# Kernel tuning notes

Hardware: AMD Instinct MI355X
Metric: run time of the kernel (lower is better)

## Reference

```python
import jax, jax.numpy as jnp
import numpy as np

DIM=2048; NH=16; QK_NOPE=128; QK_ROPE=64; QK_HD=QK_NOPE+QK_ROPE; V_HD=128
Q_LORA=1536; KV_LORA=512
IDX_NH=16; IDX_HD=128; IDX_TOPK=1024
B=1; S=2048
NEG=-1e30  # finite stand-in for -inf mask

def _hadamard(n):
    H=np.array([[1.0]],dtype=np.float32)
    while H.shape[0]<n:
        H=np.block([[H,H],[H,-H]])
    return H
_H=jnp.asarray(_hadamard(IDX_HD),jnp.bfloat16)  # symmetric Sylvester Hadamard

def _rope_tables(s,d):
    inv=1.0/(10000.0**(np.arange(0,d,2)/float(d)))
    ang=np.outer(np.arange(s),inv)
    return jnp.asarray(np.cos(ang),jnp.float32),jnp.asarray(np.sin(ang),jnp.float32)

def _rope_interleaved(x,cos,sin):
    # pairs (x[2i], x[2i+1]); x: (b,s,h,d), cos/sin: (s,d//2)
    x1=x[...,0::2]; x2=x[...,1::2]
    c=cos[None,:,None,:]; s_=sin[None,:,None,:]
    return jnp.stack([x1*c-x2*s_,x1*s_+x2*c],axis=-1).reshape(x.shape)

def _rope_half(x,cos,sin):
    # non-interleaved: pairs (x[i], x[i+d/2])
    d=x.shape[-1]//2
    x1=x[...,:d]; x2=x[...,d:]
    c=cos[None,:,None,:]; s_=sin[None,:,None,:]
    return jnp.concatenate([x1*c-x2*s_,x1*s_+x2*c],axis=-1)

def _rms(x,w,eps=1e-6):
    xf=x.astype(jnp.float32)
    xf=xf*jax.lax.rsqrt(jnp.mean(xf*xf,axis=-1,keepdims=True)+eps)
    return (w*xf).astype(x.dtype)

def _ln(x,w,b,eps=1e-6):
    xf=x.astype(jnp.float32)
    mu=jnp.mean(xf,axis=-1,keepdims=True)
    var=jnp.mean((xf-mu)**2,axis=-1,keepdims=True)
    return ((xf-mu)*jax.lax.rsqrt(var+eps)*w+b).astype(x.dtype)

def _rotate(x):
    # rotate_activation: bf16 Hadamard transform, x @ H * d^-0.5 (H symmetric)
    return (x.astype(jnp.bfloat16)@_H)*(IDX_HD**-0.5)

def _forward(x,start_pos,freqs_cos,freqs_sin,mask,q_a_proj,q_a_ln_w,q_b_proj,kv_a_proj,kv_a_ln_w,kv_b_proj,o_proj,idx_wq_b,idx_wk,idx_knorm_w,idx_knorm_b,idx_weights_proj):
    b,s,_=x.shape  # start_pos==0 prefill -> cache slice == current k/kv
    sm_scale=QK_HD**-0.5
    qr=_rms(x@q_a_proj.T,q_a_ln_w)                       # (b,s,q_lora)
    q=(qr@q_b_proj.T).reshape(b,s,NH,QK_HD)
    q_nope=q[...,:QK_NOPE]
    q_pe=_rope_interleaved(q[...,QK_NOPE:],freqs_cos,freqs_sin)
    kvp=x@kv_a_proj.T
    kv=_rms(kvp[...,:KV_LORA],kv_a_ln_w)                 # latent kv cache (b,t,c)
    k_pe=_rope_interleaved(kvp[...,KV_LORA:][:,:,None,:],freqs_cos,freqs_sin)[:,:,0,:]
    # ---------- Indexer ----------
    iq=(qr@idx_wq_b.T).reshape(b,s,IDX_NH,IDX_HD)
    iq=jnp.concatenate([_rope_half(iq[...,:QK_ROPE],freqs_cos,freqs_sin),iq[...,QK_ROPE:]],axis=-1)
    ik=_ln(x@idx_wk.T,idx_knorm_w,idx_knorm_b)           # (b,s,IDX_HD)
    ik=jnp.concatenate([_rope_half(ik[:,:,None,:QK_ROPE],freqs_cos,freqs_sin)[:,:,0,:],ik[...,QK_ROPE:]],axis=-1)
    iq=_rotate(iq); ik=_rotate(ik)                       # bf16 Hadamard-rotated
    iw=(x@idx_weights_proj.T)*(IDX_NH**-0.5)             # (b,s,hI)
    wq=(iw[...,None]*iq.astype(jnp.float32)*(IDX_HD**-0.5)).astype(jnp.bfloat16)
    sc=jnp.einsum('bshd,btd->bsht',wq,ik,preferred_element_type=jnp.float32)
    index_score=jax.nn.relu(sc).sum(axis=2)+mask[None]   # bf16_index: relu, head-sum
    _,topk=jax.lax.top_k(index_score,min(IDX_TOPK,s))    # (b,s,K)
    imask=jnp.full((b,s,s),jnp.float32(NEG))
    imask=imask.at[jnp.arange(b)[:,None,None],jnp.arange(s)[None,:,None],topk].set(0.0)
    imask=imask+mask[None]
    # ---------- Latent attention (absorbed) ----------
    wkv=kv_b_proj.reshape(NH,QK_NOPE+V_HD,KV_LORA)
    q_abs=jnp.einsum('bshd,hdc->bshc',q_nope,wkv[:,:QK_NOPE])
    scores=(jnp.einsum('bshc,btc->bsht',q_abs,kv)+jnp.einsum('bshr,btr->bsht',q_pe,k_pe))*sm_scale
    scores=scores+imask[:,:,None,:]
    p=jax.nn.softmax(scores.astype(jnp.float32),axis=-1).astype(x.dtype)
    o=jnp.einsum('bsht,btc->bshc',p,kv)
    o=jnp.einsum('bshc,hdc->bshd',o,wkv[:,QK_NOPE:])
    return o.reshape(b,s,NH*V_HD)@o_proj.T

def setup_inputs():
    key=jax.random.key(0)
    ks=jax.random.split(key,10)
    def w(k,shape):
        return jax.random.normal(k,shape,jnp.float32)*(shape[-1]**-0.5)
    cos,sin=_rope_tables(S,QK_ROPE)
    causal=jnp.where(jnp.triu(jnp.ones((S,S),bool),1),jnp.float32(NEG),jnp.float32(0.0))
    return {
        'x':jax.random.normal(ks[0],(B,S,DIM),jnp.float32),
        'start_pos':0,
        'freqs_cos':cos,'freqs_sin':sin,'mask':causal,
        'q_a_proj':w(ks[1],(Q_LORA,DIM)),
        'q_a_ln_w':jnp.ones((Q_LORA,),jnp.float32),
        'q_b_proj':w(ks[2],(NH*QK_HD,Q_LORA)),
        'kv_a_proj':w(ks[3],(KV_LORA+QK_ROPE,DIM)),
        'kv_a_ln_w':jnp.ones((KV_LORA,),jnp.float32),
        'kv_b_proj':w(ks[4],(NH*(QK_NOPE+V_HD),KV_LORA)),
        'o_proj':w(ks[5],(DIM,NH*V_HD)),
        'idx_wq_b':w(ks[6],(IDX_NH*IDX_HD,Q_LORA)),
        'idx_wk':w(ks[7],(IDX_HD,DIM)),
        'idx_knorm_w':jnp.ones((IDX_HD,),jnp.float32),
        'idx_knorm_b':jnp.zeros((IDX_HD,),jnp.float32),
        'idx_weights_proj':w(ks[8],(IDX_NH,DIM)),
    }

def reference(x,start_pos,freqs_cos,freqs_sin,mask,q_a_proj,q_a_ln_w,q_b_proj,kv_a_proj,kv_a_ln_w,kv_b_proj,o_proj,idx_wq_b,idx_wk,idx_knorm_w,idx_knorm_b,idx_weights_proj):
    return _forward(x,start_pos,freqs_cos,freqs_sin,mask,q_a_proj,q_a_ln_w,q_b_proj,kv_a_proj,kv_a_ln_w,kv_b_proj,o_proj,idx_wq_b,idx_wk,idx_knorm_w,idx_knorm_b,idx_weights_proj)
```

## Files before the change

kernel.cpp:

```cpp
#include <hip/hip_runtime.h>
#include <hip/hip_bf16.h>
#include <math.h>

#define S 2048
#define NH 16
#define DIM 2048
#define QK_NOPE 128
#define QK_ROPE 64
#define QK_HD 192
#define V_HD 128
#define Q_LORA 1536
#define KV_LORA 512
#define IDX_HD 128
#define SM_SCALE 0.07216878364870323f
#define SCHUNK 512
#define PADK 40
#define XPLD 2256
#define QLD 5120
#define XPLD_PAD 2304

typedef __hip_bfloat16 bf16;
typedef unsigned short ushort_t;
typedef __attribute__((ext_vector_type(8))) short short8;
typedef __attribute__((ext_vector_type(4))) float f32x4;

__device__ __forceinline__ f32x4 mfma_bf16(short8 a, short8 b, f32x4 c) {
    return __builtin_amdgcn_mfma_f32_16x16x32_bf16(a, b, c, 0, 0, 0);
}
__device__ __forceinline__ void async16(const void* g, void* l) {
    __builtin_amdgcn_global_load_lds((const __attribute__((address_space(1))) void*)g,
                                     (__attribute__((address_space(3))) void*)l, 16, 0, 0);
}
__device__ __forceinline__ unsigned short f2bf(float f) {
    unsigned int u = __float_as_uint(f);
    return (unsigned short)((u + 0x7fff + ((u >> 16) & 1)) >> 16);
}
__device__ __forceinline__ float bf2f(unsigned short b) {
    return __uint_as_float(((unsigned int)b) << 16);
}

__global__ __launch_bounds__(256) void split_kernel(const float* __restrict__ in, ushort_t* __restrict__ hi,
                                                    ushort_t* __restrict__ lo, int n4) {
    int idx = blockIdx.x * 256 + threadIdx.x;
    if (idx >= n4) return;
    float4 v = ((const float4*)in)[idx];
    ushort4 h, l;
    h.x = f2bf(v.x); l.x = f2bf(v.x - bf2f(h.x));
    h.y = f2bf(v.y); l.y = f2bf(v.y - bf2f(h.y));
    h.z = f2bf(v.z); l.z = f2bf(v.z - bf2f(h.z));
    h.w = f2bf(v.w); l.w = f2bf(v.w - bf2f(h.w));
    ((ushort4*)hi)[idx] = h;
    ((ushort4*)lo)[idx] = l;
}

__global__ __launch_bounds__(256) void gemm3_lds(const ushort_t* __restrict__ Ah, const ushort_t* __restrict__ Al,
                                                 const ushort_t* __restrict__ Bh, const ushort_t* __restrict__ Bl,
                                                 float* __restrict__ C, int M, int N, int K) {
    __shared__ ushort_t sAh[128 * 32], sAl[128 * 32], sBh[128 * 32], sBl[128 * 32];
    const int tid = threadIdx.x;
    const int bm = blockIdx.y * 128, bn = blockIdx.x * 128;
    const int w = tid >> 6, lane = tid & 63;
    const int wm = (w >> 1) * 64, wn = (w & 1) * 64;
    const int fr = lane & 15, fk = (lane >> 4) * 8;
    const int srow = tid >> 2, skc = (tid & 3) * 8;
    f32x4 acc[4][4];
    for (int i = 0; i < 4; ++i)
        for (int j = 0; j < 4; ++j) acc[i][j] = f32x4{0.f, 0.f, 0.f, 0.f};
    const ushort_t* pAh0 = Ah + (size_t)(bm + srow) * K + skc;
    const ushort_t* pAh1 = Ah + (size_t)(bm + 64 + srow) * K + skc;
    const ushort_t* pAl0 = Al + (size_t)(bm + srow) * K + skc;
    const ushort_t* pAl1 = Al + (size_t)(bm + 64 + srow) * K + skc;
    const ushort_t* pBh0 = Bh + (size_t)(bn + srow) * K + skc;
    const ushort_t* pBh1 = Bh + (size_t)(bn + 64 + srow) * K + skc;
    const ushort_t* pBl0 = Bl + (size_t)(bn + srow) * K + skc;
    const ushort_t* pBl1 = Bl + (size_t)(bn + 64 + srow) * K + skc;
    ushort_t* dA0 = &sAh[srow * 32 + skc];
    ushort_t* dA1 = &sAh[(64 + srow) * 32 + skc];
    ushort_t* dAl0 = &sAl[srow * 32 + skc];
    ushort_t* dAl1 = &sAl[(64 + srow) * 32 + skc];
    ushort_t* dB0 = &sBh[srow * 32 + skc];
    ushort_t* dB1 = &sBh[(64 + srow) * 32 + skc];
    ushort_t* dBl0 = &sBl[srow * 32 + skc];
    ushort_t* dBl1 = &sBl[(64 + srow) * 32 + skc];
    for (int k0 = 0; k0 < K; k0 += 32) {
        __syncthreads();
        async16(pAh0, dA0);  async16(pAh1, dA1);
        async16(pAl0, dAl0); async16(pAl1, dAl1);
        async16(pBh0, dB0);  async16(pBh1, dB1);
        async16(pBl0, dBl0); async16(pBl1, dBl1);
        pAh0 += 32; pAh1 += 32; pAl0 += 32; pAl1 += 32;
        pBh0 += 32; pBh1 += 32; pBl0 += 32; pBl1 += 32;
        __syncthreads();
        short8 ahf[4], alf[4], bhf[4], blf[4];
        for (int i = 0; i < 4; ++i) {
            int ro = (wm + i * 16 + fr) * 32 + fk;
            ahf[i] = *(const short8*)&sAh[ro];
            alf[i] = *(const short8*)&sAl[ro];
        }
        for (int j = 0; j < 4; ++j) {
            int ro = (wn + j * 16 + fr) * 32 + fk;
            bhf[j] = *(const short8*)&sBh[ro];
            blf[j] = *(const short8*)&sBl[ro];
        }
        for (int i = 0; i < 4; ++i)
            for (int j = 0; j < 4; ++j) {
                acc[i][j] = mfma_bf16(ahf[i], bhf[j], acc[i][j]);
                acc[i][j] = mfma_bf16(ahf[i], blf[j], acc[i][j]);
                acc[i][j] = mfma_bf16(alf[i], bhf[j], acc[i][j]);
            }
    }
    const int cr = (lane >> 4) * 4, cc = lane & 15;
    for (int i = 0; i < 4; ++i)
        for (int j = 0; j < 4; ++j) {
            int row = bm + wm + i * 16 + cr;
            int col = bn + wn + j * 16 + cc;
            if (col < N)
                for (int r = 0; r < 4; ++r)
                    C[(size_t)(row + r) * N + col] = acc[i][j][r];
        }
}

__global__ __launch_bounds__(256) void rms_kernel(const float* __restrict__ in, float* __restrict__ out,
                                                  const float* __restrict__ w, int C, int ldin, int ldout) {
    const int row = blockIdx.x;
    const float* xr = in + (size_t)row * ldin;
    float* yr = out + (size_t)row * ldout;
    float ss = 0.f;
    for (int c = threadIdx.x; c < C; c += 256) { float v = xr[c]; ss += v * v; }
    for (int o = 32; o; o >>= 1) ss += __shfl_down(ss, o, 64);
    __shared__ float red[4];
    const int wave = threadIdx.x >> 6, lane = threadIdx.x & 63;
    if (lane == 0) red[wave] = ss;
    __syncthreads();
    const float tot = red[0] + red[1] + red[2] + red[3];
    const float scale = rsqrtf(tot / (float)C + 1e-6f);
    for (int c = threadIdx.x; c < C; c += 256) yr[c] = w[c] * (xr[c] * scale);
}

__global__ __launch_bounds__(256) void rms_split_kernel(const float* __restrict__ in, ushort_t* __restrict__ hi,
                                                        ushort_t* __restrict__ lo, const float* __restrict__ w,
                                                        int C, int ldin) {
    const int row = blockIdx.x;
    const float* xr = in + (size_t)row * ldin;
    float ss = 0.f;
    for (int c = threadIdx.x; c < C; c += 256) { float v = xr[c]; ss += v * v; }
    for (int o = 32; o; o >>= 1) ss += __shfl_down(ss, o, 64);
    __shared__ float red[4];
    const int wave = threadIdx.x >> 6, lane = threadIdx.x & 63;
    if (lane == 0) red[wave] = ss;
    __syncthreads();
    const float tot = red[0] + red[1] + red[2] + red[3];
    const float scale = rsqrtf(tot / (float)C + 1e-6f);
    for (int c = threadIdx.x; c < C; c += 256) {
        float v = w[c] * (xr[c] * scale);
        unsigned short h = f2bf(v);
        hi[(size_t)row * C + c] = h;
        lo[(size_t)row * C + c] = f2bf(v - bf2f(h));
    }
}

__global__ __launch_bounds__(128) void ln_kernel(float* __restrict__ x, const float* __restrict__ w,
                                                 const float* __restrict__ b, int ld) {
    const int row = blockIdx.x;
    float* xr = x + (size_t)row * ld;
    const int tid = threadIdx.x;
    float v = xr[tid];
    float sm = v;
    for (int o = 32; o; o >>= 1) sm += __shfl_down(sm, o, 64);
    __shared__ float red[2];
    if ((tid & 63) == 0) red[tid >> 6] = sm;
    __syncthreads();
    const float mu = (red[0] + red[1]) * (1.f / 128.f);
    __syncthreads();
    float d = v - mu;
    float sv = d * d;
    for (int o = 32; o; o >>= 1) sv += __shfl_down(sv, o, 64);
    if ((tid & 63) == 0) red[tid >> 6] = sv;
    __syncthreads();
    const float var = (red[0] + red[1]) * (1.f / 128.f);
    const float rs = rsqrtf(var + 1e-6f);
    xr[tid] = (v - mu) * rs * w[tid] + b[tid];
}

__global__ __launch_bounds__(256) void rope_inter_kernel(float* __restrict__ X, const float* __restrict__ ct,
                                                         const float* __restrict__ st, int H, int hs, int off,
                                                         int ld) {
    int idx = blockIdx.x * 256 + threadIdx.x;
    int k = idx & 31;
    int h = (idx >> 5) % H;
    int s = idx / (32 * H);
    if (s >= S) return;
    float c = ct[s * 32 + k], sn = st[s * 32 + k];
    float* p = X + (size_t)s * ld + h * hs + off;
    float x1 = p[2 * k], x2 = p[2 * k + 1];
    p[2 * k]     = x1 * c - x2 * sn;
    p[2 * k + 1] = x1 * sn + x2 * c;
}

__global__ __launch_bounds__(256) void rope_half_kernel(float* __restrict__ X, const float* __restrict__ ct,
                                                        const float* __restrict__ st, int H, int hs, int ld) {
    int idx = blockIdx.x * 256 + threadIdx.x;
    int k = idx & 31;
    int h = (idx >> 5) % H;
    int s = idx / (32 * H);
    if (s >= S) return;
    float c = ct[s * 32 + k], sn = st[s * 32 + k];
    float* p = X + (size_t)s * ld + h * hs;
    float x1 = p[k], x2 = p[32 + k];
    p[k]      = x1 * c - x2 * sn;
    p[32 + k] = x1 * sn + x2 * c;
}

__global__ __launch_bounds__(128) void rotate_kernel(const float* __restrict__ in, int lds, int H,
                                                     bf16* __restrict__ out) {
    __shared__ float xs[128];
    const int r = blockIdx.x, j = threadIdx.x;
    const int s = r / H, h = r - s * H;
    float v = in[(size_t)s * lds + h * 128 + j];
    xs[j] = __bfloat162float(__float2bfloat16(v));
    __syncthreads();
    float acc = 0.f;
    for (int d = 0; d < 128; ++d) {
        float xv = xs[d];
        acc += (__popc(d & j) & 1) ? -xv : xv;
    }
    float t = __bfloat162float(__float2bfloat16(acc)) * 0.08838834764831845f;
    out[(size_t)r * 128 + j] = __float2bfloat16(t);
}

__global__ __launch_bounds__(256) void wq_kernel(const float* __restrict__ iwb, bf16* __restrict__ iqr) {
    int idx = blockIdx.x * 256 + threadIdx.x;
    int s = idx >> 11, h = (idx >> 7) & 15;
    float a = 0.25f * iwb[(size_t)s * XPLD + h];
    float v = __bfloat162float(iqr[idx]);
    float t = (a * v) * 0.08838834764831845f;
    iqr[idx] = __float2bfloat16(t);
}

__global__ __launch_bounds__(256) void iscore_mfma(const bf16* __restrict__ wq, const bf16* __restrict__ ik,
                                                   float* __restrict__ out) {
    if (blockIdx.x > blockIdx.y) return;
    __shared__ unsigned short As[128 * 32], Bs[128 * 32];
    const int bs = blockIdx.y * 128, bt = blockIdx.x * 128;
    const int tid = threadIdx.x, w = tid >> 6, lane = tid & 63;
    const int wm = (w >> 1) * 64, wn = (w & 1) * 64;
    const int fr = lane & 15, fk = (lane >> 4) * 8;
    const int srow = lane >> 2, skc = (lane & 3) * 8;
    f32x4 sum[4][4];
    for (int i = 0; i < 4; ++i)
        for (int j = 0; j < 4; ++j) sum[i][j] = f32x4{0.f, 0.f, 0.f, 0.f};
    for (int h = 0; h < 16; ++h) {
        f32x4 acc[4][4];
        for (int i = 0; i < 4; ++i)
            for (int j = 0; j < 4; ++j) acc[i][j] = f32x4{0.f, 0.f, 0.f, 0.f};
        for (int k0 = 0; k0 < 128; k0 += 32) {
            __syncthreads();
            for (int i = 0; i < 2; ++i) {
                int seg = i * 4 + w;
                async16(wq + (size_t)(bs + seg * 16 + srow) * 2048 + h * 128 + k0 + skc, &As[seg * 512]);
                async16(ik + (size_t)(bt + seg * 16 + srow) * 128 + k0 + skc, &Bs[seg * 512]);
            }
            __syncthreads();
            short8 af[4], bff[4];
            for (int i = 0; i < 4; ++i) af[i]  = *(const short8*)&As[(wm + i * 16 + fr) * 32 + fk];
            for (int j = 0; j < 4; ++j) bff[j] = *(const short8*)&Bs[(wn + j * 16 + fr) * 32 + fk];
            for (int i = 0; i < 4; ++i)
                for (int j = 0; j < 4; ++j)
                    acc[i][j] = mfma_bf16(af[i], bff[j], acc[i][j]);
        }
        for (int i = 0; i < 4; ++i)
            for (int j = 0; j < 4; ++j)
                for (int r = 0; r < 4; ++r)
                    sum[i][j][r] += fmaxf(acc[i][j][r], 0.f);
    }
    const int cr = (lane >> 4) * 4, cc = lane & 15;
    for (int i = 0; i < 4; ++i)
        for (int j = 0; j < 4; ++j)
            for (int r = 0; r < 4; ++r)
                out[(size_t)(bs + wm + i * 16 + cr + r) * 2048 + bt + wn + j * 16 + cc] = sum[i][j][r];
}

__global__ __launch_bounds__(256) void topk_kernel(const float* __restrict__ isc, int* __restrict__ tk) {
    __shared__ unsigned long long keys[2048];
    const int s = blockIdx.x;
    const float* row = isc + (size_t)s * 2048;
    for (int t = threadIdx.x; t < 2048; t += 256) {
        unsigned long long kk = 0ull;
        if (t <= s) {
            unsigned int vb = __float_as_uint(row[t]);
            kk = ((unsigned long long)vb << 32) | (unsigned int)(2048 - t);
        }
        keys[t] = kk;
    }
    __syncthreads();
    for (int k = 2; k <= 2048; k <<= 1) {
        for (int j = k >> 1; j > 0; j >>= 1) {
            for (int t = threadIdx.x; t < 2048; t += 256) {
                int l = t ^ j;
                if (l > t) {
                    bool up = ((t & k) == 0);
                    unsigned long long a = keys[t], b = keys[l];
                    bool sw = up ? (a < b) : (a > b);
                    if (sw) { keys[t] = b; keys[l] = a; }
                }
            }
            __syncthreads();
        }
    }
    const int cnt = min(1024, s + 1);
    for (int i = threadIdx.x; i < 1024; i += 256) {
        int t = (i < cnt) ? (2048 - (int)(keys[i] & 0xFFFFFFFFull)) : -1;
        tk[(size_t)s * 1024 + i] = t;
    }
}

__global__ __launch_bounds__(256) void w1t_kernel(const float* __restrict__ kv_b, float* __restrict__ w1t) {
    __shared__ float ts[64][65];
    const int cb = blockIdx.x * 64, db = blockIdx.y * 64, h = blockIdx.z;
    const int t = threadIdx.x;
    for (int it = 0; it < 16; ++it) {
        int idx = it * 256 + t;
        int rr = idx >> 6, cc = idx & 63;
        ts[rr][cc] = kv_b[(size_t)(h * 256 + db + rr) * 512 + cb + cc];
    }
    __syncthreads();
    for (int it = 0; it < 16; ++it) {
        int idx = it * 256 + t;
        int rr = idx >> 6, cc = idx & 63;
        w1t[(size_t)h * 65536 + (size_t)(cb + rr) * 128 + db + cc] = ts[cc][rr];
    }
}

__global__ __launch_bounds__(576) void kvsplit_kernel(const float* __restrict__ kv, const float* __restrict__ kpe,
                                                      ushort_t* __restrict__ kvh, ushort_t* __restrict__ kvl) {
    const int t = blockIdx.x, c = threadIdx.x;
    float v = (c < 512) ? kv[(size_t)t * 512 + c] : kpe[(size_t)t * XPLD + c];
    unsigned short hi = f2bf(v);
    kvh[(size_t)t * 576 + c] = hi;
    kvl[(size_t)t * 576 + c] = f2bf(v - bf2f(hi));
}

__global__ __launch_bounds__(256) void qabs_mfma(const float* __restrict__ q, const float* __restrict__ w1t,
                                                 ushort_t* __restrict__ qah, ushort_t* __restrict__ qal) {
    __shared__ unsigned short Ah[128 * PADK], Al[128 * PADK], Bh[128 * PADK], Bl[128 * PADK];
    const int tid = threadIdx.x;
    const int bn = blockIdx.x * 128, bm = blockIdx.y * 128, h = blockIdx.z;
    const int w = tid >> 6, lane = tid & 63;
    const int wm = (w >> 1) * 64, wn = (w & 1) * 64;
    const int fr = lane & 15, fk = (lane >> 4) * 8;
    f32x4 acc[4][4];
    for (int i = 0; i < 4; ++i)
        for (int j = 0; j < 4; ++j) acc[i][j] = f32x4{0.f, 0.f, 0.f, 0.f};
    for (int k0 = 0; k0 < 128; k0 += 32) {
        __syncthreads();
        for (int it = 0; it < 4; ++it) {
            int f = it * 256 + tid;
            int row = f >> 3, kc = (f & 7) * 4;
            float4 av = *(const float4*)(q + (size_t)(bm + row) * QLD + h * QK_HD + k0 + kc);
            float4 bv = *(const float4*)(w1t + (size_t)h * 65536 + (size_t)(bn + row) * 128 + k0 + kc);
            ushort4 ahi, alo, bhi, blo;
            ahi.x = f2bf(av.x); alo.x = f2bf(av.x - bf2f(ahi.x));
            ahi.y = f2bf(av.y); alo.y = f2bf(av.y - bf2f(ahi.y));
            ahi.z = f2bf(av.z); alo.z = f2bf(av.z - bf2f(ahi.z));
            ahi.w = f2bf(av.w); alo.w = f2bf(av.w - bf2f(ahi.w));
            bhi.x = f2bf(bv.x); blo.x = f2bf(bv.x - bf2f(bhi.x));
            bhi.y = f2bf(bv.y); blo.y = f2bf(bv.y - bf2f(bhi.y));
            bhi.z = f2bf(bv.z); blo.z = f2bf(bv.z - bf2f(bhi.z));
            bhi.w = f2bf(bv.w); blo.w = f2bf(bv.w - bf2f(bhi.w));
            *(ushort4*)&Ah[row * PADK + kc] = ahi;
            *(ushort4*)&Al[row * PADK + kc] = alo;
            *(ushort4*)&Bh[row * PADK + kc] = bhi;
            *(ushort4*)&Bl[row * PADK + kc] = blo;
        }
        __syncthreads();
        short8 ahf[4], alf[4], bhf[4], blf[4];
        for (int i = 0; i < 4; ++i) {
            int ro = (wm + i * 16 + fr) * PADK + fk;
            ahf[i] = *(const short8*)&Ah[ro];
            alf[i] = *(const short8*)&Al[ro];
        }
        for (int j = 0; j < 4; ++j) {
            int ro = (wn + j * 16 + fr) * PADK + fk;
            bhf[j] = *(const short8*)&Bh[ro];
            blf[j] = *(const short8*)&Bl[ro];
        }
        for (int i = 0; i < 4; ++i)
            for (int j = 0; j < 4; ++j) {
                acc[i][j] = mfma_bf16(ahf[i], bhf[j], acc[i][j]);
                acc[i][j] = mfma_bf16(ahf[i], blf[j], acc[i][j]);
                acc[i][j] = mfma_bf16(alf[i], bhf[j], acc[i][j]);
            }
    }
    const int cr = (lane >> 4) * 4, cc = lane & 15;
    for (int i = 0; i < 4; ++i)
        for (int j = 0; j < 4; ++j)
            for (int r = 0; r < 4; ++r) {
                int srow = bm + wm + i * 16 + cr + r;
                int col = bn + wn + j * 16 + cc;
                float f = acc[i][j][r] * SM_SCALE;
                size_t addr = ((size_t)srow * 16 + h) * 576 + col;
                unsigned short hi = f2bf(f);
                qah[addr] = hi;
                qal[addr] = f2bf(f - bf2f(hi));
            }
}

__global__ __launch_bounds__(256) void qpe_split(const float* __restrict__ q, ushort_t* __restrict__ qah,
                                                 ushort_t* __restrict__ qal) {
    int idx = blockIdx.x * 256 + threadIdx.x;
    int r = idx & 63, h = (idx >> 6) & 15, s = idx >> 10;
    float f = q[(size_t)s * QLD + h * QK_HD + 128 + r] * SM_SCALE;
    size_t addr = ((size_t)s * 16 + h) * 576 + 512 + r;
    unsigned short hi = f2bf(f);
    qah[addr] = hi;
    qal[addr] = f2bf(f - bf2f(hi));
}

__global__ __launch_bounds__(512) void attn_score_mfma(const ushort_t* __restrict__ qah,
                                                       const ushort_t* __restrict__ qal,
                                                       const ushort_t* __restrict__ kvh,
                                                       const ushort_t* __restrict__ kvl,
                                                       const int* __restrict__ tk,
                                                       float* __restrict__ scb, int s0) {
    const int sl = blockIdx.x, s = s0 + sl, pass = blockIdx.y;
    const int tid = threadIdx.x, w = tid >> 6, lane = tid & 63;
    const int cnt = min(1024, s + 1);
    if (pass * 256 >= cnt) {
        for (int i = tid; i < 4096; i += 512) {
            int head = i >> 8, key = i & 255;
            scb[((size_t)sl * 16 + head) * 1024 + pass * 256 + key] = -1e30f;
        }
        return;
    }
    __shared__ int tks[256];
    __shared__ __align__(16) ushort_t kh[2][8192], kl[2][8192];
    if (tid < 256) {
        int t = tk[(size_t)s * 1024 + pass * 256 + tid];
        tks[tid] = t < 0 ? 0 : t;
    }
    __syncthreads();
    const int fr = lane & 15, g = lane >> 4;
    const size_t abase = ((size_t)s * 16 + fr) * 576 + g * 8;
    const int R0 = tid >> 2;
    const int sw = (tid & 3) ^ ((R0 >> 1) & 3);
    const size_t t0 = (size_t)tks[R0], t1 = (size_t)tks[R0 + 128];
    const ushort_t* gh0 = kvh + t0 * 576 + sw * 8;
    const ushort_t* gh1 = kvh + t1 * 576 + sw * 8;
    const ushort_t* gl0 = kvl + t0 * 576 + sw * 8;
    const ushort_t* gl1 = kvl + t1 * 576 + sw * 8;
    const int ro_a = (w * 32 + fr) * 32 + ((g ^ ((fr >> 1) & 3)) << 3);
    async16(gh0, &kh[0][w * 512]);
    async16(gh1, &kh[0][4096 + w * 512]);
    async16(gl0, &kl[0][w * 512]);
    async16(gl1, &kl[0][4096 + w * 512]);
    short8 qh = *(const short8*)(qah + abase);
    short8 ql = *(const short8*)(qal + abase);
    f32x4 acc0 = {0.f, 0.f, 0.f, 0.f}, acc1 = {0.f, 0.f, 0.f, 0.f};
    int cur = 0;
    __syncthreads();
    for (int ch = 0; ch < 18; ++ch) {
        if (ch < 17) {
            int off = (ch + 1) * 32;
            async16(gh0 + off, &kh[cur ^ 1][w * 512]);
            async16(gh1 + off, &kh[cur ^ 1][4096 + w * 512]);
            async16(gl0 + off, &kl[cur ^ 1][w * 512]);
            async16(gl1 + off, &kl[cur ^ 1][4096 + w * 512]);
        }
        short8 qhc = qh, qlc = ql;
        if (ch < 17) {
            qh = *(const short8*)(qah + abase + (ch + 1) * 32);
            ql = *(const short8*)(qal + abase + (ch + 1) * 32);
        }
        short8 bh0 = *(const short8*)&kh[cur][ro_a];
        short8 bl0 = *(const short8*)&kl[cur][ro_a];
        short8 bh1 = *(const short8*)&kh[cur][ro_a + 512];
        short8 bl1 = *(const short8*)&kl[cur][ro_a + 512];
        acc0 = mfma_bf16(qhc, bh0, acc0);
        acc0 = mfma_bf16(qhc, bl0, acc0);
        acc0 = mfma_bf16(qlc, bh0, acc0);
        acc1 = mfma_bf16(qhc, bh1, acc1);
        acc1 = mfma_bf16(qhc, bl1, acc1);
        acc1 = mfma_bf16(qlc, bh1, acc1);
        __syncthreads();
        cur ^= 1;
    }
    const int cr = (lane >> 4) * 4, cc = lane & 15;
    for (int r = 0; r < 4; ++r) {
        int head = cr + r;
        int key0 = pass * 256 + w * 32 + cc;
        int key1 = key0 + 16;
        scb[((size_t)sl * 16 + head) * 1024 + key0] = (key0 < cnt) ? acc0[r] : -1e30f;
        scb[((size_t)sl * 16 + head) * 1024 + key1] = (key1 < cnt) ? acc1[r] : -1e30f;
    }
}

__global__ __launch_bounds__(256) void softmax_pb(const float* __restrict__ scb,
                                                  ushort_t* __restrict__ pbh, ushort_t* __restrict__ pbl) {
    const size_t row = blockIdx.x;
    const float* src = scb + row * 1024;
    const int tid = threadIdx.x, wave = tid >> 6, lane = tid & 63;
    __shared__ float red[4];
    float v[4];
    float m = -INFINITY;
    for (int i = 0; i < 4; ++i) { v[i] = src[tid + 256 * i]; m = fmaxf(m, v[i]); }
    for (int o = 32; o; o >>= 1) m = fmaxf(m, __shfl_down(m, o, 64));
    if (lane == 0) red[wave] = m;
    __syncthreads();
    m = fmaxf(fmaxf(red[0], red[1]), fmaxf(red[2], red[3]));
    __syncthreads();
    float e[4], l = 0.f;
    for (int i = 0; i < 4; ++i) { e[i] = __expf(v[i] - m); l += e[i]; }
    for (int o = 32; o; o >>= 1) l += __shfl_down(l, o, 64);
    if (lane == 0) red[wave] = l;
    __syncthreads();
    const float il = 1.f / (red[0] + red[1] + red[2] + red[3]);
    for (int i = 0; i < 4; ++i) {
        float p = e[i] * il;
        unsigned short hi = f2bf(p);
        pbh[row * 1024 + tid + 256 * i] = hi;
        pbl[row * 1024 + tid + 256 * i] = f2bf(p - bf2f(hi));
    }
}

__global__ __launch_bounds__(512) void attn_pv_mfma(const ushort_t* __restrict__ pbh,
                                                    const ushort_t* __restrict__ pbl,
                                                    const float* __restrict__ kv,
                                                    const int* __restrict__ tk,
                                                    float* __restrict__ o1, int s0) {
    const int sl = blockIdx.x, s = s0 + sl;
    const int tid = threadIdx.x, w = tid >> 6, lane = tid & 63;
    __shared__ int tks[1024];
    __shared__ float vt[32 * 514];
    for (int j = tid; j < 1024; j += 512) {
        int t = tk[(size_t)s * 1024 + j];
        tks[j] = t < 0 ? 0 : t;
    }
    const int fr = lane & 15, fko = (lane >> 4) * 8;
    f32x4 acc[4];
    for (int i = 0; i < 4; ++i) acc[i] = f32x4{0.f, 0.f, 0.f, 0.f};
    const size_t pbase = ((size_t)sl * 16 + fr) * 1024 + fko;
    for (int kc = 0; kc < 32; ++kc) {
        __syncthreads();
        for (int it = 0; it < 8; ++it) {
            int task = it * 512 + tid;
            int rrow = task >> 7, c4 = task & 127;
            *(float4*)&vt[rrow * 514 + c4 * 4] =
                *(const float4*)(kv + (size_t)tks[kc * 32 + rrow] * 512 + c4 * 4);
        }
        __syncthreads();
        short8 ph = *(const short8*)(pbh + pbase + kc * 32);
        short8 pl = *(const short8*)(pbl + pbase + kc * 32);
        for (int sub = 0; sub < 4; ++sub) {
            int cbase = w * 64 + sub * 16 + fr;
            short8 bh, bl;
            for (int jj = 0; jj < 8; ++jj) {
                float vv = vt[(fko + jj) * 514 + cbase];
                unsigned short hv = f2bf(vv);
                bh[jj] = (short)hv;
                bl[jj] = (short)f2bf(vv - bf2f(hv));
            }
            acc[sub] = mfma_bf16(ph, bh, acc[sub]);
            acc[sub] = mfma_bf16(pl, bh, acc[sub]);
            acc[sub] = mfma_bf16(ph, bl, acc[sub]);
        }
    }
    const int cr = (lane >> 4) * 4, cc = lane & 15;
    for (int sub = 0; sub < 4; ++sub)
        for (int r = 0; r < 4; ++r) {
            int head = cr + r, c = w * 64 + sub * 16 + cc;
            o1[((size_t)sl * 16 + head) * 512 + c] = acc[sub][r];
        }
}

__global__ __launch_bounds__(256) void outproj_mfma(const float* __restrict__ o1, const float* __restrict__ kv_b,
                                                    ushort_t* __restrict__ o2h, ushort_t* __restrict__ o2l,
                                                    int s0) {
    __shared__ unsigned short Ah[128 * PADK], Al[128 * PADK], Bh[128 * PADK], Bl[128 * PADK];
    const int tid = threadIdx.x;
    const int bm = blockIdx.y * 128, h = blockIdx.z;
    const int w = tid >> 6, lane = tid & 63;
    const int wm = (w >> 1) * 64, wn = (w & 1) * 64;
    const int fr = lane & 15, fk = (lane >> 4) * 8;
    f32x4 acc[4][4];
    for (int i = 0; i < 4; ++i)
        for (int j = 0; j < 4; ++j) acc[i][j] = f32x4{0.f, 0.f, 0.f, 0.f};
    for (int k0 = 0; k0 < 512; k0 += 32) {
        __syncthreads();
        for (int it = 0; it < 4; ++it) {
            int f = it * 256 + tid;
            int row = f >> 3, kc = (f & 7) * 4;
            float4 av = *(const float4*)(o1 + ((size_t)(bm + row) * 16 + h) * 512 + k0 + kc);
            float4 bv = *(const float4*)(kv_b + (size_t)(h * 256 + 128 + row) * 512 + k0 + kc);
            ushort4 ahi, alo, bhi, blo;
            ahi.x = f2bf(av.x); alo.x = f2bf(av.x - bf2f(ahi.x));
            ahi.y = f2bf(av.y); alo.y = f2bf(av.y - bf2f(ahi.y));
            ahi.z = f2bf(av.z); alo.z = f2bf(av.z - bf2f(ahi.z));
            ahi.w = f2bf(av.w); alo.w = f2bf(av.w - bf2f(ahi.w));
            bhi.x = f2bf(bv.x); blo.x = f2bf(bv.x - bf2f(bhi.x));
            bhi.y = f2bf(bv.y); blo.y = f2bf(bv.y - bf2f(bhi.y));
            bhi.z = f2bf(bv.z); blo.z = f2bf(bv.z - bf2f(bhi.z));
            bhi.w = f2bf(bv.w); blo.w = f2bf(bv.w - bf2f(bhi.w));
            *(ushort4*)&Ah[row * PADK + kc] = ahi;
            *(ushort4*)&Al[row * PADK + kc] = alo;
            *(ushort4*)&Bh[row * PADK + kc] = bhi;
            *(ushort4*)&Bl[row * PADK + kc] = blo;
        }
        __syncthreads();
        short8 ahf[4], alf[4], bhf[4], blf[4];
        for (int i = 0; i < 4; ++i) {
            int ro = (wm + i * 16 + fr) * PADK + fk;
            ahf[i] = *(const short8*)&Ah[ro];
            alf[i] = *(const short8*)&Al[ro];
        }
        for (int j = 0; j < 4; ++j) {
            int ro = (wn + j * 16 + fr) * PADK + fk;
            bhf[j] = *(const short8*)&Bh[ro];
            blf[j] = *(const short8*)&Bl[ro];
        }
        for (int i = 0; i < 4; ++i)
            for (int j = 0; j < 4; ++j) {
                acc[i][j] = mfma_bf16(ahf[i], bhf[j], acc[i][j]);
                acc[i][j] = mfma_bf16(ahf[i], blf[j], acc[i][j]);
                acc[i][j] = mfma_bf16(alf[i], bhf[j], acc[i][j]);
            }
    }
    const int cr = (lane >> 4) * 4, cc = lane & 15;
    for (int i = 0; i < 4; ++i)
        for (int j = 0; j < 4; ++j)
            for (int r = 0; r < 4; ++r) {
                int srow = s0 + bm + wm + i * 16 + cr + r;
                int col = wn + j * 16 + cc;
                size_t addr = (size_t)srow * 2048 + h * 128 + col;
                float f = acc[i][j][r];
                unsigned short hv = f2bf(f);
                o2h[addr] = hv;
                o2l[addr] = f2bf(f - bf2f(hv));
            }
}

extern "C" void kernel_launch(void* const* d_in, const int* in_sizes, int n_in,
                              void* d_out, int out_size, void* d_ws, size_t ws_size,
                              hipStream_t stream) {
    const float* x         = (const float*)d_in[0];
    const float* fcos      = (const float*)d_in[2];
    const float* fsin      = (const float*)d_in[3];
    const float* q_a_proj  = (const float*)d_in[5];
    const float* q_a_ln_w  = (const float*)d_in[6];
    const float* q_b_proj  = (const float*)d_in[7];
    const float* kv_a_proj = (const float*)d_in[8];
    const float* kv_a_ln_w = (const float*)d_in[9];
    const float* kv_b      = (const float*)d_in[10];
    const float* o_proj    = (const float*)d_in[11];
    const float* idx_wq_b  = (const float*)d_in[12];
    const float* idx_wk    = (const float*)d_in[13];
    const float* iknw      = (const float*)d_in[14];
    const float* iknb      = (const float*)d_in[15];
    const float* idx_wp    = (const float*)d_in[16];
    float* out = (float*)d_out;

    char* ws = (char*)d_ws;
    size_t off = 0;
    auto alloc = [&](size_t bytes) {
        char* p = ws + off;
        off += (bytes + 255) & ~(size_t)255;
        return p;
    };
    float* xp  = (float*)alloc((size_t)S * XPLD * 4);
    ushort_t* qrh = (ushort_t*)alloc((size_t)S * Q_LORA * 2);
    ushort_t* qrl = (ushort_t*)alloc((size_t)S * Q_LORA * 2);
    float* qib = (float*)alloc((size_t)S * QLD * 4);
    char* RAt  = alloc(31457280);
    float* isc = (float*)RAt;
    bf16* iqr  = (bf16*)(RAt + 16777216);
    bf16* ikr  = (bf16*)(RAt + 16777216 + 8388608);
    ushort_t* xh = (ushort_t*)RAt;
    ushort_t* xl = xh + (size_t)S * DIM;
    ushort_t* wq2h = (ushort_t*)RAt;
    ushort_t* wq2l = wq2h + (size_t)5120 * Q_LORA;
    float* w1t = (float*)RAt;
    ushort_t* wpackh = (ushort_t*)qib;
    ushort_t* wpackl = wpackh + (size_t)XPLD_PAD * DIM;
    const size_t CHUNK_BYTES = (size_t)SCHUNK * 16 * 1024 * 4 + (size_t)SCHUNK * 16 * 1024 * 2 * 2
                             + (size_t)SCHUNK * 16 * 512 * 4;
    if (off < CHUNK_BYTES) off = (CHUNK_BYTES + 255) & ~(size_t)255;
    int* tk        = (int*)alloc((size_t)S * 1024 * 4);
    float* kv      = (float*)alloc((size_t)S * KV_LORA * 4);
    ushort_t* o2h  = (ushort_t*)alloc((size_t)S * 2048 * 2);
    ushort_t* o2l  = (ushort_t*)alloc((size_t)S * 2048 * 2);
    ushort_t* qah  = (ushort_t*)alloc((size_t)S * 16 * 576 * 2);
    ushort_t* qal  = (ushort_t*)alloc((size_t)S * 16 * 576 * 2);
    ushort_t* kvh  = (ushort_t*)alloc((size_t)S * 576 * 2);
    ushort_t* kvl  = (ushort_t*)alloc((size_t)S * 576 * 2);
    float* scb    = (float*)ws;
    ushort_t* pbh = (ushort_t*)(ws + (size_t)SCHUNK * 16 * 1024 * 4);
    ushort_t* pbl = pbh + (size_t)SCHUNK * 16 * 1024;
    float* o1c    = (float*)(ws + (size_t)SCHUNK * 16 * 1024 * 8);
    ushort_t* oph = (ushort_t*)ws;
    ushort_t* opl = oph + (size_t)DIM * 2048;

    split_kernel<<<S * DIM / 1024, 256, 0, stream>>>(x, xh, xl, S * DIM / 4);
    split_kernel<<<Q_LORA * DIM / 1024, 256, 0, stream>>>(q_a_proj, wpackh, wpackl, Q_LORA * DIM / 4);
    split_kernel<<<576 * DIM / 1024, 256, 0, stream>>>(kv_a_proj, wpackh + (size_t)1536 * DIM,
                                                       wpackl + (size_t)1536 * DIM, 576 * DIM / 4);
    split_kernel<<<128 * DIM / 1024, 256, 0, stream>>>(idx_wk, wpackh + (size_t)2112 * DIM,
                                                       wpackl + (size_t)2112 * DIM, 128 * DIM / 4);
    split_kernel<<<16 * DIM / 1024, 256, 0, stream>>>(idx_wp, wpackh + (size_t)2240 * DIM,
                                                      wpackl + (size_t)2240 * DIM, 16 * DIM / 4);
    hipMemsetAsync(wpackh + (size_t)XPLD * DIM, 0, (size_t)(XPLD_PAD - XPLD) * DIM * 2, stream);
    hipMemsetAsync(wpackl + (size_t)XPLD * DIM, 0, (size_t)(XPLD_PAD - XPLD) * DIM * 2, stream);
    gemm3_lds<<<dim3((XPLD + 127) / 128, S / 128), 256, 0, stream>>>(xh, xl, wpackh, wpackl, xp, S, XPLD, DIM);
    rms_split_kernel<<<S, 256, 0, stream>>>(xp, qrh, qrl, q_a_ln_w, Q_LORA, XPLD);
    rms_kernel<<<S, 256, 0, stream>>>(xp + 1536, kv, kv_a_ln_w, KV_LORA, XPLD, KV_LORA);
    split_kernel<<<3072 * Q_LORA / 1024, 256, 0, stream>>>(q_b_proj, wq2h, wq2l, 3072 * Q_LORA / 4);
    split_kernel<<<2048 * Q_LORA / 1024, 256, 0, stream>>>(idx_wq_b, wq2h + (size_t)3072 * Q_LORA,
                                                           wq2l + (size_t)3072 * Q_LORA, 2048 * Q_LORA / 4);
    gemm3_lds<<<dim3(QLD / 128, S / 128), 256, 0, stream>>>(qrh, qrl, wq2h, wq2l, qib, S, QLD, Q_LORA);
    rope_inter_kernel<<<S * NH * 32 / 256, 256, 0, stream>>>(qib, fcos, fsin, NH, QK_HD, QK_NOPE, QLD);
    rope_inter_kernel<<<S * 32 / 256, 256, 0, stream>>>(xp + 1536, fcos, fsin, 1, 0, KV_LORA, XPLD);
    rope_half_kernel<<<S * NH * 32 / 256, 256, 0, stream>>>(qib + 3072, fcos, fsin, NH, 128, QLD);
    ln_kernel<<<S, 128, 0, stream>>>(xp + 2112, iknw, iknb, XPLD);
    rope_half_kernel<<<S * 32 / 256, 256, 0, stream>>>(xp + 2112, fcos, fsin, 1, 0, XPLD);
    rotate_kernel<<<S * NH, 128, 0, stream>>>(qib + 3072, QLD, NH, iqr);
    rotate_kernel<<<S, 128, 0, stream>>>(xp + 2112, XPLD, 1, ikr);
    wq_kernel<<<S * NH * 128 / 256, 256, 0, stream>>>(xp + 2240, iqr);
    iscore_mfma<<<dim3(16, 16), 256, 0, stream>>>(iqr, ikr, isc);
    topk_kernel<<<S, 256, 0, stream>>>(isc, tk);
    w1t_kernel<<<dim3(8, 2, 16), 256, 0, stream>>>(kv_b, w1t);
    kvsplit_kernel<<<S, 576, 0, stream>>>(kv, xp + 1536, kvh, kvl);
    qabs_mfma<<<dim3(4, S / 128, 16), 256, 0, stream>>>(qib, w1t, qah, qal);
    qpe_split<<<S * NH * 64 / 256, 256, 0, stream>>>(qib, qah, qal);
    for (int c = 0; c < 4; ++c) {
        int s0 = c * SCHUNK;
        attn_score_mfma<<<dim3(SCHUNK, 4), 512, 0, stream>>>(qah, qal, kvh, kvl, tk, scb, s0);
        softmax_pb<<<SCHUNK * 16, 256, 0, stream>>>(scb, pbh, pbl);
        attn_pv_mfma<<<SCHUNK, 512, 0, stream>>>(pbh, pbl, kv, tk, o1c, s0);
        outproj_mfma<<<dim3(1, 4, 16), 256, 0, stream>>>(o1c, kv_b, o2h, o2l, s0);
    }
    split_kernel<<<DIM * 2048 / 1024, 256, 0, stream>>>(o_proj, oph, opl, DIM * 2048 / 4);
    gemm3_lds<<<dim3(DIM / 128, S / 128), 256, 0, stream>>>(o2h, o2l, oph, opl, out, S, DIM, NH * V_HD);
}
```

Measured before the change: 1.875 ms.

## Pre-split latent KV and W2 to bf16 pairs, prefetch PV gathers, async outproj loads

```diff
diff --git a/kernel.cpp b/kernel.cpp
--- a/kernel.cpp
+++ b/kernel.cpp
@@ -51,6 +51,21 @@
     h.w = f2bf(v.w); l.w = f2bf(v.w - bf2f(h.w));
     ((ushort4*)hi)[idx] = h;
     ((ushort4*)lo)[idx] = l;
+}
+
+__global__ __launch_bounds__(256) void splitw2_kernel(const float* __restrict__ kv_b,
+                                                      ushort_t* __restrict__ w2h, ushort_t* __restrict__ w2l) {
+    int idx = blockIdx.x * 256 + threadIdx.x;
+    int h = idx >> 14, rem = idx & 16383;
+    int row = rem >> 7, c4 = (rem & 127) * 4;
+    float4 v = *(const float4*)(kv_b + ((size_t)(h * 256 + 128 + row)) * 512 + c4);
+    ushort4 hh, ll;
+    hh.x = f2bf(v.x); ll.x = f2bf(v.x - bf2f(hh.x));
+    hh.y = f2bf(v.y); ll.y = f2bf(v.y - bf2f(hh.y));
+    hh.z = f2bf(v.z); ll.z = f2bf(v.z - bf2f(hh.z));
+    hh.w = f2bf(v.w); ll.w = f2bf(v.w - bf2f(hh.w));
+    *(ushort4*)(w2h + ((size_t)(h * 128 + row)) * 512 + c4) = hh;
+    *(ushort4*)(w2l + ((size_t)(h * 128 + row)) * 512 + c4) = ll;
 }
 
 __global__ __launch_bounds__(256) void gemm3_lds(const ushort_t* __restrict__ Ah, const ushort_t* __restrict__ Al,
@@ -332,12 +347,15 @@
 }
 
 __global__ __launch_bounds__(576) void kvsplit_kernel(const float* __restrict__ kv, const float* __restrict__ kpe,
-                                                      ushort_t* __restrict__ kvh, ushort_t* __restrict__ kvl) {
+                                                      ushort_t* __restrict__ kvh, ushort_t* __restrict__ kvl,
+                                                      unsigned int* __restrict__ kvi) {
     const int t = blockIdx.x, c = threadIdx.x;
     float v = (c < 512) ? kv[(size_t)t * 512 + c] : kpe[(size_t)t * XPLD + c];
     unsigned short hi = f2bf(v);
+    unsigned short lo = f2bf(v - bf2f(hi));
     kvh[(size_t)t * 576 + c] = hi;
-    kvl[(size_t)t * 576 + c] = f2bf(v - bf2f(hi));
+    kvl[(size_t)t * 576 + c] = lo;
+    if (c < 512) kvi[(size_t)t * 512 + c] = (unsigned int)hi | ((unsigned int)lo << 16);
 }
 
 __global__ __launch_bounds__(256) void qabs_mfma(const float* __restrict__ q, const float* __restrict__ w1t,
@@ -524,98 +542,134 @@
 
 __global__ __launch_bounds__(512) void attn_pv_mfma(const ushort_t* __restrict__ pbh,
                                                     const ushort_t* __restrict__ pbl,
-                                                    const float* __restrict__ kv,
+                                                    const unsigned int* __restrict__ kvi,
                                                     const int* __restrict__ tk,
-                                                    float* __restrict__ o1, int s0) {
+                                                    ushort_t* __restrict__ o1h, ushort_t* __restrict__ o1l,
+                                                    int s0) {
     const int sl = blockIdx.x, s = s0 + sl;
     const int tid = threadIdx.x, w = tid >> 6, lane = tid & 63;
     __shared__ int tks[1024];
-    __shared__ float vt[32 * 514];
+    __shared__ unsigned int vt[32 * 512];
     for (int j = tid; j < 1024; j += 512) {
         int t = tk[(size_t)s * 1024 + j];
         tks[j] = t < 0 ? 0 : t;
     }
-    const int fr = lane & 15, fko = (lane >> 4) * 8;
+    const int fr = lane & 15, g = lane >> 4, fko = g * 8;
+    const int r0 = tid >> 7;
+    const int gp = tid & 127;
     f32x4 acc[4];
     for (int i = 0; i < 4; ++i) acc[i] = f32x4{0.f, 0.f, 0.f, 0.f};
     const size_t pbase = ((size_t)sl * 16 + fr) * 1024 + fko;
+    __syncthreads();
+    uint4 stg[8];
+    #pragma unroll
+    for (int it = 0; it < 8; ++it) {
+        const int r = it * 4 + r0;
+        stg[it] = *(const uint4*)(kvi + (size_t)tks[r] * 512 + (size_t)gp * 4);
+    }
+    #pragma unroll
+    for (int it = 0; it < 8; ++it) {
+        const int r = it * 4 + r0;
+        *(uint4*)&vt[r * 512 + ((gp ^ ((r >> 3) << 1)) << 2)] = stg[it];
+    }
+    __syncthreads();
     for (int kc = 0; kc < 32; ++kc) {
-        __syncthreads();
-        for (int it = 0; it < 8; ++it) {
-            int task = it * 512 + tid;
-            int rrow = task >> 7, c4 = task & 127;
-            *(float4*)&vt[rrow * 514 + c4 * 4] =
-                *(const float4*)(kv + (size_t)tks[kc * 32 + rrow] * 512 + c4 * 4);
-        }
-        __syncthreads();
+        if (kc < 31) {
+            #pragma unroll
+            for (int it = 0; it < 8; ++it) {
+                const int r = it * 4 + r0;
+                stg[it] = *(const uint4*)(kvi + (size_t)tks[(kc + 1) * 32 + r] * 512 + (size_t)gp * 4);
+            }
+        }
         short8 ph = *(const short8*)(pbh + pbase + kc * 32);
         short8 pl = *(const short8*)(pbl + pbase + kc * 32);
+        #pragma unroll
         for (int sub = 0; sub < 4; ++sub) {
-            int cbase = w * 64 + sub * 16 + fr;
+            const int cb = (w * 64 + sub * 16 + fr) ^ (g << 3);
             short8 bh, bl;
+            #pragma unroll
             for (int jj = 0; jj < 8; ++jj) {
-                float vv = vt[(fko + jj) * 514 + cbase];
-                unsigned short hv = f2bf(vv);
-                bh[jj] = (short)hv;
-                bl[jj] = (short)f2bf(vv - bf2f(hv));
+                const unsigned int v = vt[(fko + jj) * 512 + cb];
+                bh[jj] = (short)(v & 0xffffu);
+                bl[jj] = (short)(v >> 16);
             }
             acc[sub] = mfma_bf16(ph, bh, acc[sub]);
             acc[sub] = mfma_bf16(pl, bh, acc[sub]);
             acc[sub] = mfma_bf16(ph, bl, acc[sub]);
+        }
+        __syncthreads();
+        if (kc < 31) {
+            #pragma unroll
+            for (int it = 0; it < 8; ++it) {
+                const int r = it * 4 + r0;
+                *(uint4*)&vt[r * 512 + ((gp ^ ((r >> 3) << 1)) << 2)] = stg[it];
+            }
+            __syncthreads();
         }
     }
     const int cr = (lane >> 4) * 4, cc = lane & 15;
     for (int sub = 0; sub < 4; ++sub)
         for (int r = 0; r < 4; ++r) {
             int head = cr + r, c = w * 64 + sub * 16 + cc;
-            o1[((size_t)sl * 16 + head) * 512 + c] = acc[sub][r];
-        }
-}
-
-__global__ __launch_bounds__(256) void outproj_mfma(const float* __restrict__ o1, const float* __restrict__ kv_b,
+            float f = acc[sub][r];
+            unsigned short hv = f2bf(f);
+            size_t addr = ((size_t)sl * 16 + head) * 512 + c;
+            o1h[addr] = hv;
+            o1l[addr] = f2bf(f - bf2f(hv));
+        }
+}
+
+__global__ __launch_bounds__(256) void outproj_mfma(const ushort_t* __restrict__ o1h,
+                                                    const ushort_t* __restrict__ o1l,
+                                                    const ushort_t* __restrict__ w2h,
+                                                    const ushort_t* __restrict__ w2l,
                                                     ushort_t* __restrict__ o2h, ushort_t* __restrict__ o2l,
                                                     int s0) {
-    __shared__ unsigned short Ah[128 * PADK], Al[128 * PADK], Bh[128 * PADK], Bl[128 * PADK];
+    __shared__ ushort_t sAh[128 * 32], sAl[128 * 32], sBh[128 * 32], sBl[128 * 32];
     const int tid = threadIdx.x;
-    const int bm = blockIdx.y * 128, h = blockIdx.z;
+    const int bm = blockIdx.x * 128, h = blockIdx.y;
     const int w = tid >> 6, lane = tid & 63;
     const int wm = (w >> 1) * 64, wn = (w & 1) * 64;
     const int fr = lane & 15, fk = (lane >> 4) * 8;
+    const int srow = tid >> 2, skc = (tid & 3) * 8;
     f32x4 acc[4][4];
     for (int i = 0; i < 4; ++i)
         for (int j = 0; j < 4; ++j) acc[i][j] = f32x4{0.f, 0.f, 0.f, 0.f};
+    const ushort_t* pAh0 = o1h + ((size_t)(bm + srow) * 16 + h) * 512 + skc;
+    const ushort_t* pAh1 = o1h + ((size_t)(bm + 64 + srow) * 16 + h) * 512 + skc;
+    const ushort_t* pAl0 = o1l + ((size_t)(bm + srow) * 16 + h) * 512 + skc;
+    const ushort_t* pAl1 = o1l + ((size_t)(bm + 64 + srow) * 16 + h) * 512 + skc;
+    const ushort_t* pBh0 = w2h + ((size_t)(h * 128 + srow)) * 512 + skc;
+    const ushort_t* pBh1 = w2h + ((size_t)(h * 128 + 64 + srow)) * 512 + skc;
+    const ushort_t* pBl0 = w2l + ((size_t)(h * 128 + srow)) * 512 + skc;
+    const ushort_t* pBl1 = w2l + ((size_t)(h * 128 + 64 + srow)) * 512 + skc;
+    ushort_t* dA0 = &sAh[srow * 32 + skc];
+    ushort_t* dA1 = &sAh[(64 + srow) * 32 + skc];
+    ushort_t* dAl0 = &sAl[srow * 32 + skc];
+    ushort_t* dAl1 = &sAl[(64 + srow) * 32 + skc];
+    ushort_t* dB0 = &sBh[srow * 32 + skc];
+    ushort_t* dB1 = &sBh[(64 + srow) * 32 + skc];
+    ushort_t* dBl0 = &sBl[srow * 32 + skc];
+    ushort_t* dBl1 = &sBl[(64 + srow) * 32 + skc];
     for (int k0 = 0; k0 < 512; k0 += 32) {
         __syncthreads();
-        for (int it = 0; it < 4; ++it) {
-            int f = it * 256 + tid;
-            int row = f >> 3, kc = (f & 7) * 4;
-            float4 av = *(const float4*)(o1 + ((size_t)(bm + row) * 16 + h) * 512 + k0 + kc);
-            float4 bv = *(const float4*)(kv_b + (size_t)(h * 256 + 128 + row) * 512 + k0 + kc);
-            ushort4 ahi, alo, bhi, blo;
-            ahi.x = f2bf(av.x); alo.x = f2bf(av.x - bf2f(ahi.x));
-            ahi.y = f2bf(av.y); alo.y = f2bf(av.y - bf2f(ahi.y));
-            ahi.z = f2bf(av.z); alo.z = f2bf(av.z - bf2f(ahi.z));
-            ahi.w = f2bf(av.w); alo.w = f2bf(av.w - bf2f(ahi.w));
-            bhi.x = f2bf(bv.x); blo.x = f2bf(bv.x - bf2f(bhi.x));
-            bhi.y = f2bf(bv.y); blo.y = f2bf(bv.y - bf2f(bhi.y));
-            bhi.z = f2bf(bv.z); blo.z = f2bf(bv.z - bf2f(bhi.z));
-            bhi.w = f2bf(bv.w); blo.w = f2bf(bv.w - bf2f(bhi.w));
-            *(ushort4*)&Ah[row * PADK + kc] = ahi;
-            *(ushort4*)&Al[row * PADK + kc] = alo;
-            *(ushort4*)&Bh[row * PADK + kc] = bhi;
-            *(ushort4*)&Bl[row * PADK + kc] = blo;
-        }
+        async16(pAh0, dA0);  async16(pAh1, dA1);
+        async16(pAl0, dAl0); async16(pAl1, dAl1);
+        async16(pBh0, dB0);  async16(pBh1, dB1);
+        async16(pBl0, dBl0); async16(pBl1, dBl1);
+        pAh0 += 32; pAh1 += 32; pAl0 += 32; pAl1 += 32;
+        pBh0 += 32; pBh1 += 32; pBl0 += 32; pBl1 += 32;
         __syncthreads();
         short8 ahf[4], alf[4], bhf[4], blf[4];
         for (int i = 0; i < 4; ++i) {
-            int ro = (wm + i * 16 + fr) * PADK + fk;
-            ahf[i] = *(const short8*)&Ah[ro];
-            alf[i] = *(const short8*)&Al[ro];
+            int ro = (wm + i * 16 + fr) * 32 + fk;
+            ahf[i] = *(const short8*)&sAh[ro];
+            alf[i] = *(const short8*)&sAl[ro];
         }
         for (int j = 0; j < 4; ++j) {
-            int ro = (wn + j * 16 + fr) * PADK + fk;
-            bhf[j] = *(const short8*)&Bh[ro];
-            blf[j] = *(const short8*)&Bl[ro];
+            int ro = (wn + j * 16 + fr) * 32 + fk;
+            bhf[j] = *(const short8*)&sBh[ro];
+            blf[j] = *(const short8*)&sBl[ro];
         }
         for (int i = 0; i < 4; ++i)
             for (int j = 0; j < 4; ++j) {
@@ -628,9 +682,9 @@
     for (int i = 0; i < 4; ++i)
         for (int j = 0; j < 4; ++j)
             for (int r = 0; r < 4; ++r) {
-                int srow = s0 + bm + wm + i * 16 + cr + r;
+                int srow2 = s0 + bm + wm + i * 16 + cr + r;
                 int col = wn + j * 16 + cc;
-                size_t addr = (size_t)srow * 2048 + h * 128 + col;
+                size_t addr = (size_t)srow2 * 2048 + h * 128 + col;
                 float f = acc[i][j][r];
                 unsigned short hv = f2bf(f);
                 o2h[addr] = hv;
@@ -680,6 +734,10 @@
     float* w1t = (float*)RAt;
     ushort_t* wpackh = (ushort_t*)qib;
     ushort_t* wpackl = wpackh + (size_t)XPLD_PAD * DIM;
+    char* kvtail = RAt + (size_t)22 * 1024 * 1024;
+    unsigned int* kvi = (unsigned int*)kvtail;
+    ushort_t* w2h = (ushort_t*)(kvtail + (size_t)4 * 1024 * 1024);
+    ushort_t* w2l = w2h + (size_t)16 * 128 * 512;
     const size_t CHUNK_BYTES = (size_t)SCHUNK * 16 * 1024 * 4 + (size_t)SCHUNK * 16 * 1024 * 2 * 2
                              + (size_t)SCHUNK * 16 * 512 * 4;
     if (off < CHUNK_BYTES) off = (CHUNK_BYTES + 255) & ~(size_t)255;
@@ -694,7 +752,8 @@
     float* scb    = (float*)ws;
     ushort_t* pbh = (ushort_t*)(ws + (size_t)SCHUNK * 16 * 1024 * 4);
     ushort_t* pbl = pbh + (size_t)SCHUNK * 16 * 1024;
-    float* o1c    = (float*)(ws + (size_t)SCHUNK * 16 * 1024 * 8);
+    ushort_t* o1h = (ushort_t*)(ws + (size_t)SCHUNK * 16 * 1024 * 8);
+    ushort_t* o1l = o1h + (size_t)SCHUNK * 16 * 512;
     ushort_t* oph = (ushort_t*)ws;
     ushort_t* opl = oph + (size_t)DIM * 2048;
 
@@ -726,15 +785,16 @@
     iscore_mfma<<<dim3(16, 16), 256, 0, stream>>>(iqr, ikr, isc);
     topk_kernel<<<S, 256, 0, stream>>>(isc, tk);
     w1t_kernel<<<dim3(8, 2, 16), 256, 0, stream>>>(kv_b, w1t);
-    kvsplit_kernel<<<S, 576, 0, stream>>>(kv, xp + 1536, kvh, kvl);
     qabs_mfma<<<dim3(4, S / 128, 16), 256, 0, stream>>>(qib, w1t, qah, qal);
     qpe_split<<<S * NH * 64 / 256, 256, 0, stream>>>(qib, qah, qal);
+    kvsplit_kernel<<<S, 576, 0, stream>>>(kv, xp + 1536, kvh, kvl, kvi);
+    splitw2_kernel<<<1024, 256, 0, stream>>>(kv_b, w2h, w2l);
     for (int c = 0; c < 4; ++c) {
         int s0 = c * SCHUNK;
         attn_score_mfma<<<dim3(SCHUNK, 4), 512, 0, stream>>>(qah, qal, kvh, kvl, tk, scb, s0);
         softmax_pb<<<SCHUNK * 16, 256, 0, stream>>>(scb, pbh, pbl);
-        attn_pv_mfma<<<SCHUNK, 512, 0, stream>>>(pbh, pbl, kv, tk, o1c, s0);
-        outproj_mfma<<<dim3(1, 4, 16), 256, 0, stream>>>(o1c, kv_b, o2h, o2l, s0);
+        attn_pv_mfma<<<SCHUNK, 512, 0, stream>>>(pbh, pbl, kvi, tk, o1h, o1l, s0);
+        outproj_mfma<<<dim3(4, 16), 256, 0, stream>>>(o1h, o1l, w2h, w2l, o2h, o2l, s0);
     }
     split_kernel<<<DIM * 2048 / 1024, 256, 0, stream>>>(o_proj, oph, opl, DIM * 2048 / 4);
     gemm3_lds<<<dim3(DIM / 128, S / 128), 256, 0, stream>>>(o2h, o2l, oph, opl, out, S, DIM, NH * V_HD);
```

After: 2.787 ms. 48.6% more time.
